# Kernel optimization log

Hardware: AMD Instinct MI355X
Metric: run time of the kernel (lower is better)

## Reference

```python
import jax, jax.numpy as jnp
import numpy as np

M = 8      # number of modalities (len(ModalityType))
D = 256    # embedding_dim
B = 8192   # batch size


def setup_inputs() -> dict:
    key = jax.random.key(0)
    ks = jax.random.split(key, 12)
    s = 1.0 / np.sqrt(D)
    x = jax.random.normal(ks[0], (M, B, D), dtype=jnp.float32)
    reasoning_query = jax.random.normal(ks[1], (B, D), dtype=jnp.float32)
    # Per ordered modality pair (src, tgt): seq_len=1 MHA reduces to out_proj(V_proj(tgt)).
    Wv = jax.random.normal(ks[2], (M, M, D, D), dtype=jnp.float32) * s
    bv = jnp.zeros((M, M, D), dtype=jnp.float32)
    Wo = jax.random.normal(ks[3], (M, M, D, D), dtype=jnp.float32) * s
    bo = jnp.zeros((M, M, D), dtype=jnp.float32)
    # Per-modality fusion MLP: Linear(2D->D), ReLU, Linear(D->D)  (dropout = eval/identity)
    W1 = jax.random.normal(ks[4], (M, D, 2 * D), dtype=jnp.float32) * s
    b1 = jnp.zeros((M, D), dtype=jnp.float32)
    W2 = jax.random.normal(ks[5], (M, D, D), dtype=jnp.float32) * s
    b2 = jnp.zeros((M, D), dtype=jnp.float32)
    # Attention controller: Linear(2D->D), ReLU, Linear(D->1), Sigmoid
    Wc1 = jax.random.normal(ks[6], (D, 2 * D), dtype=jnp.float32) * s
    bc1 = jnp.zeros((D,), dtype=jnp.float32)
    wc2 = jax.random.normal(ks[7], (D,), dtype=jnp.float32) * s
    bc2 = jnp.zeros((1,), dtype=jnp.float32)
    return dict(x=x, reasoning_query=reasoning_query, Wv=Wv, bv=bv, Wo=Wo, bo=bo,
                W1=W1, b1=b1, W2=W2, b2=b2, Wc1=Wc1, bc1=bc1, wc2=wc2, bc2=bc2)


def reference(x, reasoning_query, Wv, bv, Wo, bo, W1, b1, W2, b2, Wc1, bc1, wc2, bc2):
    m = x.shape[0]
    # Cross-modal attention with seq_len=1: softmax over one key == 1, so the
    # attended output is exactly out_proj(V_proj(tgt_embedding)) for every pair.
    h = jnp.einsum('tbd,sted->stbe', x, Wv) + bv[:, :, None, :]          # [M,M,B,D]
    ctx = jnp.einsum('stbe,stoe->stbo', h, Wo) + bo[:, :, None, :]       # [M,M,B,D]
    # Mean over the M-1 target modalities (src != tgt), matching stack(...).mean(-1)
    offdiag = (1.0 - jnp.eye(m, dtype=x.dtype))[:, :, None, None]
    cross = (ctx * offdiag).sum(axis=1) / (m - 1)                         # [M,B,D]
    # Per-modality fusion MLP on cat([original, cross])
    comb = jnp.concatenate([x, cross], axis=-1)                           # [M,B,2D]
    hid = jax.nn.relu(jnp.einsum('mbf,mdf->mbd', comb, W1) + b1[:, None, :])
    fused = jnp.einsum('mbd,mod->mbo', hid, W2) + b2[:, None, :]          # [M,B,D]
    # Reasoning-query gating controller
    q = jnp.broadcast_to(reasoning_query[None], fused.shape)              # [M,B,D]
    qc = jnp.concatenate([q, fused], axis=-1)                             # [M,B,2D]
    ch = jax.nn.relu(jnp.einsum('mbf,df->mbd', qc, Wc1) + bc1)
    score = jax.nn.sigmoid(jnp.einsum('mbd,d->mb', ch, wc2) + bc2)        # [M,B]
    gated = fused * score[..., None]
    unified = gated.mean(axis=0)                                          # [B,D]
    return unified
```

## Files before the change

kernel.cpp:

```cpp
#include <hip/hip_runtime.h>

#define MMOD 8
#define BB 8192
#define DD 256

typedef unsigned short u16;
typedef __attribute__((ext_vector_type(8))) short s16x8;
typedef __attribute__((ext_vector_type(4))) float f32x4;
typedef __attribute__((ext_vector_type(8))) unsigned short u16x8;

typedef __attribute__((address_space(3))) unsigned short lds_u16;
typedef __attribute__((address_space(1))) const unsigned short gl_u16;

__device__ __forceinline__ float b2f(u16 u){ union{unsigned i; float f;} x; x.i=((unsigned)u)<<16; return x.f; }
__device__ __forceinline__ u16 f2b(float f){ union{float f; unsigned i;} x; x.f=f; unsigned r = x.i + 0x7FFF + ((x.i>>16)&1u); return (u16)(r>>16); }

__device__ __forceinline__ void async_cp16(const u16* g, u16* l){
  __builtin_amdgcn_global_load_lds((gl_u16*)g, (lds_u16*)l, 16, 0, 0);
}

struct ConvArgs {
  const float* src[10];
  u16*         dst[10];
  int          n[10];
};
__global__ void convert_kernel(ConvArgs a){
  const long long stride = (long long)gridDim.x * blockDim.x;
  const long long base   = (long long)blockIdx.x * blockDim.x + threadIdx.x;
  for (int s = 0; s < 10; s++){
    const int n  = a.n[s];
    const int n8 = n >> 3;
    const float* sp = a.src[s];
    u16* dst = a.dst[s];
    for (long long i = base; i < n8; i += stride){
      float4 lo = ((const float4*)sp)[i*2];
      float4 hi = ((const float4*)sp)[i*2+1];
      u16x8 p;
      p[0]=f2b(lo.x); p[1]=f2b(lo.y); p[2]=f2b(lo.z); p[3]=f2b(lo.w);
      p[4]=f2b(hi.x); p[5]=f2b(hi.y); p[6]=f2b(hi.z); p[7]=f2b(hi.w);
      *(u16x8*)(dst + (i<<3)) = p;
    }
    for (long long i = ((long long)n8<<3) + base; i < n; i += stride)
      dst[i] = f2b(sp[i]);
  }
}

__device__ __forceinline__ s16x8 load8_f32(const float* p, long long idx){
  float4 lo = *(const float4*)(p + idx);
  float4 hi = *(const float4*)(p + idx + 4);
  s16x8 r;
  r[0]=(short)f2b(lo.x); r[1]=(short)f2b(lo.y); r[2]=(short)f2b(lo.z); r[3]=(short)f2b(lo.w);
  r[4]=(short)f2b(hi.x); r[5]=(short)f2b(hi.y); r[6]=(short)f2b(hi.z); r[7]=(short)f2b(hi.w);
  return r;
}

struct GArgs {
  const u16* A;  long long a_z; long long a_piece; int lda;
  const u16* A2; long long a2_z;
  const u16* B;  long long b_z; int ldb;
  u16*       C;  long long c_z; long long c_npiece; int ldc;
  const u16* bias; long long bias_z;
  const float* cbias;
  const u16* addm;
  const u16* wc2;
  float*     scores;
  float scale;
  int K;
  int relu;
};

__global__ __launch_bounds__(256, 2) void gemm_bt(GArgs g){
  alignas(16) __shared__ u16 lA[128*64];
  alignas(16) __shared__ u16 lB[128*64];
  const int tid  = threadIdx.x;
  const int lane = tid & 63;
  const int w    = tid >> 6;
  const int z    = blockIdx.z;

  const u16* Bbase = g.B + (long long)z * g.b_z + (long long)(blockIdx.y * 128) * g.ldb;

  f32x4 acc[4][4];
  #pragma unroll
  for (int i=0;i<4;i++)
    #pragma unroll
    for (int j=0;j<4;j++)
      #pragma unroll
      for (int r=0;r<4;r++) acc[i][j][r] = 0.0f;

  const int wr = (w >> 1) * 64, wc = (w & 1) * 64;
  const int fm = lane & 15;
  const int fk = (lane >> 4) * 8;
  const long long arow0 = (long long)blockIdx.x * 128;

  const int sr = lane >> 3;
  const int sq = (lane & 7) ^ sr;

  for (int k0 = 0; k0 < g.K; k0 += 64){
    const u16* Abase0 = (g.A2 && k0 >= 256) ? (g.A2 + (long long)z * g.a2_z)
                                            : (g.A  + (long long)z * g.a_z);
    const u16* At = Abase0 + (long long)(k0 >> 8) * g.a_piece + (k0 & 255);
    const u16* Bt = Bbase + k0;
    __syncthreads();
    #pragma unroll
    for (int i=0;i<4;i++){
      int r = i*32 + w*8 + sr;
      async_cp16(At + (arow0 + r) * (long long)g.lda + sq*8, lA + (i*256 + w*64) * 8);
      async_cp16(Bt + (long long)r * g.ldb + sq*8, lB + (i*256 + w*64) * 8);
    }
    __syncthreads();
    #pragma unroll
    for (int kk = 0; kk < 64; kk += 32){
      s16x8 af[4], bfr[4];
      const int qf = (kk + fk) >> 3;
      #pragma unroll
      for (int mi=0; mi<4; mi++){
        int r = wr + mi*16 + fm;
        af[mi] = *(const s16x8*)(lA + (r*8 + (qf ^ (r & 7))) * 8);
      }
      #pragma unroll
      for (int ni=0; ni<4; ni++){
        int r = wc + ni*16 + fm;
        bfr[ni] = *(const s16x8*)(lB + (r*8 + (qf ^ (r & 7))) * 8);
      }
      #pragma unroll
      for (int mi=0; mi<4; mi++)
        #pragma unroll
        for (int ni=0; ni<4; ni++)
          acc[mi][ni] = __builtin_amdgcn_mfma_f32_16x16x32_bf16(af[mi], bfr[ni], acc[mi][ni], 0, 0, 0);
    }
  }

  u16* Cb = g.C + (long long)z * g.c_z;
  const u16* biasp = g.bias ? g.bias + (long long)z * g.bias_z : (const u16*)0;
  #pragma unroll
  for (int mi=0; mi<4; mi++){
    #pragma unroll
    for (int ni=0; ni<4; ni++){
      int n = blockIdx.y*128 + wc + ni*16 + fm;
      float bb = 0.0f;
      if (g.cbias) bb = g.cbias[n];
      else if (biasp) bb = b2f(biasp[n]);
      long long cn = ((long long)(n >> 8)) * g.c_npiece + (n & 255);
      #pragma unroll
      for (int r=0; r<4; r++){
        long long b = arow0 + wr + mi*16 + (lane>>4)*4 + r;
        float v = acc[mi][ni][r] * g.scale + bb;
        if (g.addm) v += b2f(g.addm[b*256 + n]);
        if (g.relu) v = v > 0.0f ? v : 0.0f;
        Cb[cn + b * (long long)g.ldc] = f2b(v);
      }
    }
  }
}

__global__ __launch_bounds__(256, 4) void gemm_thin(GArgs g){
  alignas(16) __shared__ u16 lA[64*64];
  alignas(16) __shared__ u16 lB[256*64];
  const int tid  = threadIdx.x;
  const int lane = tid & 63;
  const int w    = tid >> 6;
  const int z    = blockIdx.z;

  const u16* Bbase = g.B + (long long)z * g.b_z;

  f32x4 acc[16];
  #pragma unroll
  for (int j=0;j<16;j++)
    #pragma unroll
    for (int r=0;r<4;r++) acc[j][r] = 0.0f;

  const int fm = lane & 15;
  const int fk = (lane >> 4) * 8;
  const long long arow0 = (long long)blockIdx.x * 64;

  const int sr = lane >> 3;
  const int sq = (lane & 7) ^ sr;

  for (int k0 = 0; k0 < g.K; k0 += 64){
    const u16* Abase0 = (g.A2 && k0 >= 256) ? (g.A2 + (long long)z * g.a2_z)
                                            : (g.A  + (long long)z * g.a_z);
    const u16* At = Abase0 + (long long)(k0 >> 8) * g.a_piece + (k0 & 255);
    const u16* Bt = Bbase + k0;
    __syncthreads();
    #pragma unroll
    for (int i=0;i<2;i++){
      int r = i*32 + w*8 + sr;
      async_cp16(At + (arow0 + r) * (long long)g.lda + sq*8, lA + (i*256 + w*64) * 8);
    }
    #pragma unroll
    for (int i=0;i<8;i++){
      int r = i*32 + w*8 + sr;
      async_cp16(Bt + (long long)r * g.ldb + sq*8, lB + (i*256 + w*64) * 8);
    }
    __syncthreads();
    #pragma unroll
    for (int kk = 0; kk < 64; kk += 32){
      const int qf = (kk + fk) >> 3;
      int ra = w*16 + fm;
      s16x8 af = *(const s16x8*)(lA + (ra*8 + (qf ^ (ra & 7))) * 8);
      #pragma unroll
      for (int ni=0; ni<16; ni++){
        int r = ni*16 + fm;
        s16x8 bfr = *(const s16x8*)(lB + (r*8 + (qf ^ (r & 7))) * 8);
        acc[ni] = __builtin_amdgcn_mfma_f32_16x16x32_bf16(af, bfr, acc[ni], 0, 0, 0);
      }
    }
  }

  u16* Cb = g.C + (long long)z * g.c_z;
  const u16* biasp = g.bias ? g.bias + (long long)z * g.bias_z : (const u16*)0;
  #pragma unroll
  for (int ni=0; ni<16; ni++){
    int n = ni*16 + fm;
    float bb = 0.0f;
    if (g.cbias) bb = g.cbias[n];
    else if (biasp) bb = b2f(biasp[n]);
    #pragma unroll
    for (int r=0; r<4; r++){
      long long b = arow0 + w*16 + (lane>>4)*4 + r;
      float v = acc[ni][r] * g.scale + bb;
      if (g.addm) v += b2f(g.addm[b*256 + n]);
      if (g.relu) v = v > 0.0f ? v : 0.0f;
      Cb[b * (long long)g.ldc + n] = f2b(v);
    }
  }
}

__global__ __launch_bounds__(256, 4) void gemm_score(GArgs g){
  alignas(16) __shared__ u16 lA[64*64];
  alignas(16) __shared__ u16 lB[256*64];
  const int tid  = threadIdx.x;
  const int lane = tid & 63;
  const int w    = tid >> 6;
  const int z    = blockIdx.z;

  const u16* Bbase = g.B;

  f32x4 acc[16];
  #pragma unroll
  for (int j=0;j<16;j++)
    #pragma unroll
    for (int r=0;r<4;r++) acc[j][r] = 0.0f;

  const int fm = lane & 15;
  const int fk = (lane >> 4) * 8;
  const long long arow0 = (long long)blockIdx.x * 64;

  const int sr = lane >> 3;
  const int sq = (lane & 7) ^ sr;

  for (int k0 = 0; k0 < g.K; k0 += 64){
    const u16* At = g.A + (long long)z * g.a_z + k0;
    const u16* Bt = Bbase + k0;
    __syncthreads();
    #pragma unroll
    for (int i=0;i<2;i++){
      int r = i*32 + w*8 + sr;
      async_cp16(At + (arow0 + r) * (long long)g.lda + sq*8, lA + (i*256 + w*64) * 8);
    }
    #pragma unroll
    for (int i=0;i<8;i++){
      int r = i*32 + w*8 + sr;
      async_cp16(Bt + (long long)r * g.ldb + sq*8, lB + (i*256 + w*64) * 8);
    }
    __syncthreads();
    #pragma unroll
    for (int kk = 0; kk < 64; kk += 32){
      const int qf = (kk + fk) >> 3;
      int ra = w*16 + fm;
      s16x8 af = *(const s16x8*)(lA + (ra*8 + (qf ^ (ra & 7))) * 8);
      #pragma unroll
      for (int ni=0; ni<16; ni++){
        int r = ni*16 + fm;
        s16x8 bfr = *(const s16x8*)(lB + (r*8 + (qf ^ (r & 7))) * 8);
        acc[ni] = __builtin_amdgcn_mfma_f32_16x16x32_bf16(af, bfr, acc[ni], 0, 0, 0);
      }
    }
  }

  float p[4] = {0.f, 0.f, 0.f, 0.f};
  #pragma unroll
  for (int ni=0; ni<16; ni++){
    int n = ni*16 + fm;
    float bb = b2f(g.bias[n]);
    float wcv = b2f(g.wc2[n]);
    #pragma unroll
    for (int r=0; r<4; r++){
      long long b = arow0 + w*16 + (lane>>4)*4 + r;
      float v = acc[ni][r] + bb + b2f(g.addm[b*256 + n]);
      v = v > 0.0f ? v : 0.0f;
      p[r] += v * wcv;
    }
  }
  #pragma unroll
  for (int r=0; r<4; r++){
    #pragma unroll
    for (int off=1; off<16; off<<=1) p[r] += __shfl_xor(p[r], off);
  }
  if (fm == 0){
    float bc2f = g.cbias[0];
    #pragma unroll
    for (int r=0; r<4; r++){
      long long b = arow0 + w*16 + (lane>>4)*4 + r;
      g.scores[(long long)z*BB + b] = 1.0f / (1.0f + __expf(-(p[r] + bc2f)));
    }
  }
}

__global__ __launch_bounds__(256, 2) void build_wb(const float* Wo, const float* Wv, u16* WB){
  alignas(16) __shared__ u16 lA[128*64];
  alignas(16) __shared__ u16 lB[128*64];
  const int tid  = threadIdx.x;
  const int lane = tid & 63;
  const int w    = tid >> 6;
  const int z = blockIdx.z, s = z >> 3, t = z & 7;
  const long long zoff = (long long)z * 65536;

  f32x4 acc[4][4];
  #pragma unroll
  for (int i=0;i<4;i++)
    #pragma unroll
    for (int j=0;j<4;j++)
      #pragma unroll
      for (int r=0;r<4;r++) acc[i][j][r] = 0.0f;

  const int wr = (w >> 1) * 64, wc = (w & 1) * 64;
  const int fm = lane & 15;
  const int fk = (lane >> 4) * 8;

  int srow[4], sq[4];
  #pragma unroll
  for (int i=0;i<4;i++){
    int c = i*256 + tid;
    srow[i] = c >> 3;
    sq[i]   = (c & 7) ^ (srow[i] & 7);
  }

  for (int k0 = 0; k0 < 256; k0 += 64){
    s16x8 va[4], vt[4];
    #pragma unroll
    for (int i=0;i<4;i++){
      long long aidx = zoff + (long long)(blockIdx.x*128 + srow[i]) * 256 + k0 + sq[i]*8;
      va[i] = load8_f32(Wo, aidx);
    }
    #pragma unroll
    for (int j=0;j<4;j++){
      int id = j*256 + tid;
      int e  = id >> 4;
      int dc = (id & 15) * 8;
      long long bidx = zoff + (long long)(k0 + e) * 256 + blockIdx.y*128 + dc;
      vt[j] = load8_f32(Wv, bidx);
    }
    __syncthreads();
    #pragma unroll
    for (int i=0;i<4;i++){
      int c = i*256 + tid;
      *(s16x8*)(lA + c*8) = va[i];
    }
    #pragma unroll
    for (int j=0;j<4;j++){
      int id = j*256 + tid;
      int e  = id >> 4;
      int dc = (id & 15) * 8;
      #pragma unroll
      for (int u=0; u<8; u++){
        int d = dc + u;
        lB[(d*8 + ((e>>3) ^ (d & 7)))*8 + (e & 7)] = (u16)vt[j][u];
      }
    }
    __syncthreads();
    #pragma unroll
    for (int kk = 0; kk < 64; kk += 32){
      s16x8 af[4], bfr[4];
      const int qf = (kk + fk) >> 3;
      #pragma unroll
      for (int mi=0; mi<4; mi++){
        int r = wr + mi*16 + fm;
        af[mi] = *(const s16x8*)(lA + (r*8 + (qf ^ (r & 7))) * 8);
      }
      #pragma unroll
      for (int ni=0; ni<4; ni++){
        int r = wc + ni*16 + fm;
        bfr[ni] = *(const s16x8*)(lB + (r*8 + (qf ^ (r & 7))) * 8);
      }
      #pragma unroll
      for (int mi=0; mi<4; mi++)
        #pragma unroll
        for (int ni=0; ni<4; ni++)
          acc[mi][ni] = __builtin_amdgcn_mfma_f32_16x16x32_bf16(af[mi], bfr[ni], acc[mi][ni], 0, 0, 0);
    }
    __syncthreads();
  }
  const int diag = (s == t);
  #pragma unroll
  for (int mi=0; mi<4; mi++){
    #pragma unroll
    for (int ni=0; ni<4; ni++){
      int d = blockIdx.y*128 + wc + ni*16 + fm;
      #pragma unroll
      for (int r=0; r<4; r++){
        int o = blockIdx.x*128 + wr + mi*16 + (lane>>4)*4 + r;
        float v = diag ? 0.0f : acc[mi][ni][r];
        WB[(long long)(s*256 + o) * 2048 + t*256 + d] = f2b(v);
      }
    }
  }
}

__global__ __launch_bounds__(256) void cb_kernel(const float* bv, const float* Wo, const float* bo, float* cb){
  int z = blockIdx.x, s = z >> 3, t = z & 7;
  if (s == t) return;
  int lane = threadIdx.x & 63, w = threadIdx.x >> 6;
  float4 bvv = *(const float4*)(bv + (long long)z*256 + lane*4);
  #pragma unroll
  for (int i=0; i<16; i++){
    int row = blockIdx.y*64 + w*16 + i;
    float4 wv4 = *(const float4*)(Wo + (long long)z*65536 + (long long)row*256 + lane*4);
    float p = wv4.x*bvv.x + wv4.y*bvv.y + wv4.z*bvv.z + wv4.w*bvv.w;
    #pragma unroll
    for (int off=32; off>0; off>>=1) p += __shfl_xor(p, off);
    if (lane == 0)
      atomicAdd(&cb[s*256 + row], (p + bo[(long long)z*256 + row]) * (1.0f/7.0f));
  }
}

__global__ __launch_bounds__(256) void final_gate(const u16* fused, const float* scores, float* out){
  int b = blockIdx.x;
  int tid = threadIdx.x;
  float sc[8];
  #pragma unroll
  for (int m=0; m<8; m++) sc[m] = scores[(long long)m*BB + b];
  float acc = 0.0f;
  #pragma unroll
  for (int m=0; m<8; m++)
    acc += b2f(fused[((long long)m*BB + b)*256 + tid]) * sc[m];
  out[(long long)b*256 + tid] = acc * 0.125f;
}

extern "C" void kernel_launch(void* const* d_in, const int* in_sizes, int n_in,
                              void* d_out, int out_size, void* d_ws, size_t ws_size,
                              hipStream_t stream){
  const float* x   = (const float*)d_in[0];
  const float* q   = (const float*)d_in[1];
  const float* Wv  = (const float*)d_in[2];
  const float* bv  = (const float*)d_in[3];
  const float* Wo  = (const float*)d_in[4];
  const float* bo  = (const float*)d_in[5];
  const float* W1  = (const float*)d_in[6];
  const float* b1  = (const float*)d_in[7];
  const float* W2  = (const float*)d_in[8];
  const float* b2  = (const float*)d_in[9];
  const float* Wc1 = (const float*)d_in[10];
  const float* bc1 = (const float*)d_in[11];
  const float* wc2 = (const float*)d_in[12];
  const float* bc2 = (const float*)d_in[13];

  char* ws = (char*)d_ws;
  u16*   xb    = (u16*)(ws + 0LL);
  u16*   qb    = (u16*)(ws + 33554432LL);
  u16*   cross = (u16*)(ws + 37748736LL);
  u16*   hid   = (u16*)(ws + 71303168LL);
  u16*   WB    = (u16*)(ws + 104857600LL);
  u16*   W1b   = (u16*)(ws + 113246208LL);
  u16*   W2b   = (u16*)(ws + 115343360LL);
  u16*   Wc1b  = (u16*)(ws + 116391936LL);
  u16*   b1b   = (u16*)(ws + 116654080LL);
  u16*   b2b   = (u16*)(ws + 116658176LL);
  u16*   bc1b  = (u16*)(ws + 116662272LL);
  u16*   wc2b  = (u16*)(ws + 116662784LL);
  float* bc2f  = (float*)(ws + 116663296LL);
  float* cb    = (float*)(ws + 116663424LL);
  u16*   fused = xb;
  u16*   qctx  = WB;
  float* scores = (float*)(ws + 104857600LL + 4194304LL);

  ConvArgs ca{};
  ca.src[0]=x;   ca.dst[0]=xb;   ca.n[0]=MMOD*BB*DD;
  ca.src[1]=q;   ca.dst[1]=qb;   ca.n[1]=BB*DD;
  ca.src[2]=W1;  ca.dst[2]=W1b;  ca.n[2]=MMOD*DD*2*DD;
  ca.src[3]=W2;  ca.dst[3]=W2b;  ca.n[3]=MMOD*DD*DD;
  ca.src[4]=Wc1; ca.dst[4]=Wc1b; ca.n[4]=DD*2*DD;
  ca.src[5]=b1;  ca.dst[5]=b1b;  ca.n[5]=MMOD*DD;
  ca.src[6]=b2;  ca.dst[6]=b2b;  ca.n[6]=MMOD*DD;
  ca.src[7]=bc1; ca.dst[7]=bc1b; ca.n[7]=DD;
  ca.src[8]=wc2; ca.dst[8]=wc2b; ca.n[8]=DD;
  ca.src[9]=bc2; ca.dst[9]=bc1b; ca.n[9]=0;
  convert_kernel<<<1024, 256, 0, stream>>>(ca);
  hipMemcpyAsync(bc2f, bc2, sizeof(float), hipMemcpyDeviceToDevice, stream);

  hipMemsetAsync(cb, 0, 2048*sizeof(float), stream);
  build_wb<<<dim3(2,2,64), 256, 0, stream>>>(Wo, Wv, WB);
  cb_kernel<<<dim3(64,4), 256, 0, stream>>>(bv, Wo, bo, cb);

  const long long BD = (long long)BB * DD;

  GArgs g2{};
  g2.A = xb; g2.a_z = 0; g2.a_piece = BD; g2.lda = 256; g2.A2 = 0; g2.a2_z = 0;
  g2.B = WB; g2.b_z = 0; g2.ldb = 2048;
  g2.C = cross; g2.c_z = 0; g2.c_npiece = BD; g2.ldc = 256;
  g2.bias = 0; g2.bias_z = 0; g2.cbias = cb; g2.addm = 0; g2.wc2 = 0; g2.scores = 0;
  g2.scale = 1.0f/7.0f; g2.K = 2048; g2.relu = 0;
  gemm_bt<<<dim3(64,16,1), 256, 0, stream>>>(g2);

  GArgs g5a{};
  g5a.A = qb; g5a.a_z = 0; g5a.a_piece = 0; g5a.lda = 256; g5a.A2 = 0; g5a.a2_z = 0;
  g5a.B = Wc1b; g5a.b_z = 0; g5a.ldb = 512;
  g5a.C = qctx; g5a.c_z = 0; g5a.c_npiece = 0; g5a.ldc = 256;
  g5a.bias = 0; g5a.bias_z = 0; g5a.cbias = 0; g5a.addm = 0; g5a.wc2 = 0; g5a.scores = 0;
  g5a.scale = 1.0f; g5a.K = 256; g5a.relu = 0;
  gemm_thin<<<dim3(128,1,1), 256, 0, stream>>>(g5a);

  GArgs g3{};
  g3.A = xb; g3.a_z = BD; g3.a_piece = 0; g3.lda = 256; g3.A2 = cross; g3.a2_z = BD;
  g3.B = W1b; g3.b_z = (long long)DD*2*DD; g3.ldb = 512;
  g3.C = hid; g3.c_z = BD; g3.c_npiece = 0; g3.ldc = 256;
  g3.bias = b1b; g3.bias_z = 256; g3.cbias = 0; g3.addm = 0; g3.wc2 = 0; g3.scores = 0;
  g3.scale = 1.0f; g3.K = 512; g3.relu = 1;
  gemm_thin<<<dim3(128,1,8), 256, 0, stream>>>(g3);

  GArgs g4{};
  g4.A = hid; g4.a_z = BD; g4.a_piece = 0; g4.lda = 256; g4.A2 = 0; g4.a2_z = 0;
  g4.B = W2b; g4.b_z = (long long)DD*DD; g4.ldb = 256;
  g4.C = fused; g4.c_z = BD; g4.c_npiece = 0; g4.ldc = 256;
  g4.bias = b2b; g4.bias_z = 256; g4.cbias = 0; g4.addm = 0; g4.wc2 = 0; g4.scores = 0;
  g4.scale = 1.0f; g4.K = 256; g4.relu = 0;
  gemm_thin<<<dim3(128,1,8), 256, 0, stream>>>(g4);

  GArgs g5b{};
  g5b.A = fused; g5b.a_z = BD; g5b.a_piece = 0; g5b.lda = 256; g5b.A2 = 0; g5b.a2_z = 0;
  g5b.B = Wc1b + 256; g5b.b_z = 0; g5b.ldb = 512;
  g5b.C = 0; g5b.c_z = 0; g5b.c_npiece = 0; g5b.ldc = 0;
  g5b.bias = bc1b; g5b.bias_z = 0; g5b.cbias = bc2f; g5b.addm = qctx;
  g5b.wc2 = wc2b; g5b.scores = scores;
  g5b.scale = 1.0f; g5b.K = 256; g5b.relu = 1;
  gemm_score<<<dim3(128,1,8), 256, 0, stream>>>(g5b);

  final_gate<<<dim3(BB), 256, 0, stream>>>(fused, scores, (float*)d_out);

  (void)in_sizes; (void)n_in; (void)out_size; (void)ws_size;
}
```

Measured before the change: 357.2 us.

## Add 256x256-tile 8-wave pipelined GEMM for the cross-modal projection

Adds a new GEMM kernel with 512 threads and 256x256 output tiles. It double-buffers A and B in 128KB of LDS using async global-to-LDS copies, an XOR swizzle, prefetch interleaved across four compute phases, and s_setprio around the MFMA bursts. The kernel replaces gemm_bt for the large K=2048 cross-modal GEMM, aiming for more data reuse per tile and better overlap of loads with MFMA. In exchange it launches only 256 blocks, so wave occupancy is low, and the barrier-heavy schedule may stall.

```diff
diff --git a/kernel.cpp b/kernel.cpp
--- a/kernel.cpp
+++ b/kernel.cpp
@@ -153,6 +153,138 @@
   }
 }
 
+__global__ __launch_bounds__(512, 2) void gemm_8ph(GArgs g){
+  alignas(16) __shared__ u16 L[65536];
+  const int tid  = threadIdx.x;
+  const int lane = tid & 63;
+  const int w    = tid >> 6;
+  const int z    = blockIdx.z;
+
+  const int wr  = w >> 2;
+  const int wcn = w & 3;
+  const int fm  = lane & 15;
+  const int fq  = lane >> 4;
+
+  const long long arow0 = (long long)blockIdx.x * 256;
+  const long long nrow0 = (long long)blockIdx.y * 256;
+
+  const int r0  = tid >> 3;
+  const int r1  = r0 + 64;
+  const int cs  = tid & 7;
+  const int gc0 = cs ^ (r0 & 7);
+  const int gc1 = cs ^ (r1 & 7);
+  const int ldst0 = (w * 64) * 8;
+  const int ldst1 = (512 + w * 64) * 8;
+
+  const u16* Az = g.A + (long long)z * g.a_z;
+  const u16* Bz = g.B + (long long)z * g.b_z;
+
+#define STAGE_A8(c, k0s, h) do{ \
+    const u16* gb_ = Az + (long long)((k0s) >> 8) * g.a_piece + ((k0s) & 255); \
+    const long long gr_ = arow0 + (h) * 128; \
+    u16* lb_ = L + ((c) * 2 + 0) * 16384 + (h) * 8192; \
+    async_cp16(gb_ + (gr_ + r0) * (long long)g.lda + gc0 * 8, lb_ + ldst0); \
+    async_cp16(gb_ + (gr_ + r1) * (long long)g.lda + gc1 * 8, lb_ + ldst1); \
+  }while(0)
+#define STAGE_B8(c, k0s, h) do{ \
+    const u16* gb_ = Bz + (k0s); \
+    const long long gr_ = nrow0 + (h) * 128; \
+    u16* lb_ = L + ((c) * 2 + 1) * 16384 + (h) * 8192; \
+    async_cp16(gb_ + (gr_ + r0) * (long long)g.ldb + gc0 * 8, lb_ + ldst0); \
+    async_cp16(gb_ + (gr_ + r1) * (long long)g.ldb + gc1 * 8, lb_ + ldst1); \
+  }while(0)
+
+  f32x4 acc[8][4];
+  #pragma unroll
+  for (int i=0;i<8;i++)
+    #pragma unroll
+    for (int j=0;j<4;j++)
+      #pragma unroll
+      for (int r=0;r<4;r++) acc[i][j][r] = 0.0f;
+
+  const int T = g.K >> 6;
+
+  STAGE_A8(0, 0, 0);  STAGE_A8(0, 0, 1);
+  STAGE_B8(0, 0, 0);  STAGE_B8(0, 0, 1);
+  STAGE_B8(1, 64, 0); STAGE_B8(1, 64, 1);
+  asm volatile("s_waitcnt vmcnt(4)" ::: "memory");
+  __builtin_amdgcn_s_barrier();
+
+  int c = 0;
+  for (int t = 0; t < T; ++t, c ^= 1){
+    const int k0 = t << 6;
+    const u16* lA = L + (c * 2 + 0) * 16384;
+    const u16* lB = L + (c * 2 + 1) * 16384;
+    s16x8 bf[4][2];
+    #pragma unroll
+    for (int q = 0; q < 4; ++q){
+      if (q == 0 && t + 1 < T) STAGE_A8(c ^ 1, k0 + 64, 0);
+      if (q == 1 && t + 1 < T) STAGE_A8(c ^ 1, k0 + 64, 1);
+      if (q == 2 && t + 2 < T) STAGE_B8(c,     k0 + 128, 0);
+      if (q == 3 && t + 2 < T) STAGE_B8(c,     k0 + 128, 1);
+      if (q == 0){
+        #pragma unroll
+        for (int ni = 0; ni < 4; ni++){
+          const int R = wcn * 64 + ni * 16 + fm;
+          #pragma unroll
+          for (int kk = 0; kk < 2; kk++){
+            const int qf = kk * 4 + fq;
+            bf[ni][kk] = *(const s16x8*)(lB + R * 64 + ((qf ^ (R & 7)) << 3));
+          }
+        }
+      }
+      s16x8 af[2][2];
+      #pragma unroll
+      for (int j = 0; j < 2; j++){
+        const int R = wr * 128 + (q * 2 + j) * 16 + fm;
+        #pragma unroll
+        for (int kk = 0; kk < 2; kk++){
+          const int qf = kk * 4 + fq;
+          af[j][kk] = *(const s16x8*)(lA + R * 64 + ((qf ^ (R & 7)) << 3));
+        }
+      }
+      __builtin_amdgcn_s_barrier();
+      __builtin_amdgcn_s_setprio(1);
+      #pragma unroll
+      for (int kk = 0; kk < 2; kk++)
+        #pragma unroll
+        for (int j = 0; j < 2; j++)
+          #pragma unroll
+          for (int ni = 0; ni < 4; ni++)
+            acc[q*2+j][ni] = __builtin_amdgcn_mfma_f32_16x16x32_bf16(af[j][kk], bf[ni][kk], acc[q*2+j][ni], 0, 0, 0);
+      __builtin_amdgcn_s_setprio(0);
+      if (q == 3){
+        if (t + 2 < T)      asm volatile("s_waitcnt vmcnt(4)" ::: "memory");
+        else if (t + 1 < T) asm volatile("s_waitcnt vmcnt(0)" ::: "memory");
+      }
+      __builtin_amdgcn_s_barrier();
+    }
+  }
+
+  u16* Cb = g.C + (long long)z * g.c_z;
+  const u16* biasp = g.bias ? g.bias + (long long)z * g.bias_z : (const u16*)0;
+  #pragma unroll
+  for (int mi = 0; mi < 8; mi++){
+    #pragma unroll
+    for (int ni = 0; ni < 4; ni++){
+      const int n = (int)nrow0 + wcn * 64 + ni * 16 + fm;
+      float bb = 0.0f;
+      if (g.cbias) bb = g.cbias[n];
+      else if (biasp) bb = b2f(biasp[n]);
+      const long long cn = ((long long)(n >> 8)) * g.c_npiece + (n & 255);
+      #pragma unroll
+      for (int r = 0; r < 4; r++){
+        const long long b = arow0 + wr * 128 + mi * 16 + fq * 4 + r;
+        float v = acc[mi][ni][r] * g.scale + bb;
+        if (g.relu) v = v > 0.0f ? v : 0.0f;
+        Cb[cn + b * (long long)g.ldc] = f2b(v);
+      }
+    }
+  }
+#undef STAGE_A8
+#undef STAGE_B8
+}
+
 __global__ __launch_bounds__(256, 4) void gemm_thin(GArgs g){
   alignas(16) __shared__ u16 lA[64*64];
   alignas(16) __shared__ u16 lB[256*64];
@@ -500,7 +632,7 @@
   g2.C = cross; g2.c_z = 0; g2.c_npiece = BD; g2.ldc = 256;
   g2.bias = 0; g2.bias_z = 0; g2.cbias = cb; g2.addm = 0; g2.wc2 = 0; g2.scores = 0;
   g2.scale = 1.0f/7.0f; g2.K = 2048; g2.relu = 0;
-  gemm_bt<<<dim3(64,16,1), 256, 0, stream>>>(g2);
+  gemm_8ph<<<dim3(32,8,1), 512, 0, stream>>>(g2);
 
   GArgs g5a{};
   g5a.A = qb; g5a.a_z = 0; g5a.a_piece = 0; g5a.lda = 256; g5a.A2 = 0; g5a.a2_z = 0;
```

After: 364.6 us. +2.1%, slower.

## Replace cross-modal GEMM with 256x256-tile, 8-wave, double-buffered pipelined kernel

Applied to the files above, without the earlier changes.

Replaces the 128x128-tile gemm_bt used for the big cross-modal GEMM (K=2048) with a 512-thread kernel that computes 256x256 output tiles per block. The new kernel uses 128KB of LDS, double-buffered across k-tiles. Async global-to-LDS loads for the next tile are interleaved with MFMA phases using explicit vmcnt waits, barriers and s_setprio. The aim is to hide load latency and raise data reuse per block. In exchange the kernel hardcodes lda=256, ldb=2048 and z=0, drops the addm path, and launches only 256 blocks, which may leave some CUs underused.

```diff
diff --git a/kernel.cpp b/kernel.cpp
--- a/kernel.cpp
+++ b/kernel.cpp
@@ -69,88 +69,165 @@
   int relu;
 };
 
-__global__ __launch_bounds__(256, 2) void gemm_bt(GArgs g){
-  alignas(16) __shared__ u16 lA[128*64];
-  alignas(16) __shared__ u16 lB[128*64];
+__global__ __launch_bounds__(512, 2) void gemm_8ph(GArgs g){
+  alignas(16) __shared__ char L[131072];
   const int tid  = threadIdx.x;
   const int lane = tid & 63;
   const int w    = tid >> 6;
-  const int z    = blockIdx.z;
-
-  const u16* Bbase = g.B + (long long)z * g.b_z + (long long)(blockIdx.y * 128) * g.ldb;
-
-  f32x4 acc[4][4];
-  #pragma unroll
-  for (int i=0;i<4;i++)
+
+  const int wr  = w >> 2;
+  const int wcn = w & 3;
+  const int fm  = lane & 15;
+  const int fq  = lane >> 4;
+
+  const long long arow0 = (long long)blockIdx.x * 256;
+  const long long nrow0 = (long long)blockIdx.y * 256;
+
+  const int lp0 = fm*128 + (((0*4+fq) ^ (fm&7))*16);
+  const int lp1 = fm*128 + (((1*4+fq) ^ (fm&7))*16);
+  const int vA00 =          wr*16384 + lp0;
+  const int vA01 =          wr*16384 + lp1;
+  const int vA10 = 65536 +  wr*16384 + lp0;
+  const int vA11 = 65536 +  wr*16384 + lp1;
+  const int vB00 =          32768 + wcn*8192 + lp0;
+  const int vB01 =          32768 + wcn*8192 + lp1;
+  const int vB10 = 65536 +  32768 + wcn*8192 + lp0;
+  const int vB11 = 65536 +  32768 + wcn*8192 + lp1;
+
+  const int r0  = tid >> 3;
+  const int r1  = r0 + 64;
+  const int cs  = tid & 7;
+  const int gc0 = cs ^ (r0 & 7);
+  const int gc1 = cs ^ (r1 & 7);
+  const int laA0 = r0*256  + gc0*8;
+  const int laA1 = r1*256  + gc1*8;
+  const int laB0 = r0*2048 + gc0*8;
+  const int laB1 = r1*2048 + gc1*8;
+
+  const u16* Az = g.A;
+  const u16* Bz = g.B;
+
+#define STAGE_A(c, k0s, h) do{ \
+    const u16* s_ = Az + (long long)((k0s) >> 8) * g.a_piece + ((k0s) & 255) + (arow0 + (h)*128) * 256; \
+    char* d_ = L + (c)*65536 + (h)*16384 + w*1024; \
+    async_cp16(s_ + laA0, (u16*)d_); \
+    async_cp16(s_ + laA1, (u16*)(d_ + 8192)); \
+  }while(0)
+#define STAGE_B(c, k0s, h) do{ \
+    const u16* s_ = Bz + (k0s) + (nrow0 + (h)*128) * 2048; \
+    char* d_ = L + (c)*65536 + 32768 + (h)*16384 + w*1024; \
+    async_cp16(s_ + laB0, (u16*)d_); \
+    async_cp16(s_ + laB1, (u16*)(d_ + 8192)); \
+  }while(0)
+
+  s16x8 af[2][2][2];
+  s16x8 bf[4][2];
+
+#define RD_A(vb0, vb1, slot, qq) do{ \
+    af[slot][0][0] = *(const s16x8*)(L + (vb0) + ((qq)*2+0)*2048); \
+    af[slot][0][1] = *(const s16x8*)(L + (vb1) + ((qq)*2+0)*2048); \
+    af[slot][1][0] = *(const s16x8*)(L + (vb0) + ((qq)*2+1)*2048); \
+    af[slot][1][1] = *(const s16x8*)(L + (vb1) + ((qq)*2+1)*2048); \
+  }while(0)
+#define RD_B(vb0, vb1) do{ \
+    bf[0][0] = *(const s16x8*)(L + (vb0) + 0*2048); \
+    bf[0][1] = *(const s16x8*)(L + (vb1) + 0*2048); \
+    bf[1][0] = *(const s16x8*)(L + (vb0) + 1*2048); \
+    bf[1][1] = *(const s16x8*)(L + (vb1) + 1*2048); \
+    bf[2][0] = *(const s16x8*)(L + (vb0) + 2*2048); \
+    bf[2][1] = *(const s16x8*)(L + (vb1) + 2*2048); \
+    bf[3][0] = *(const s16x8*)(L + (vb0) + 3*2048); \
+    bf[3][1] = *(const s16x8*)(L + (vb1) + 3*2048); \
+  }while(0)
+
+#define MFMA_Q(qq, slot) do{ \
+    __builtin_amdgcn_s_setprio(1); \
+    _Pragma("unroll") \
+    for (int kk = 0; kk < 2; kk++) \
+      _Pragma("unroll") \
+      for (int j = 0; j < 2; j++) \
+        _Pragma("unroll") \
+        for (int ni = 0; ni < 4; ni++) \
+          acc[(qq)*2+j][ni] = __builtin_amdgcn_mfma_f32_16x16x32_bf16(af[slot][j][kk], bf[ni][kk], acc[(qq)*2+j][ni], 0, 0, 0); \
+    __builtin_amdgcn_s_setprio(0); \
+  }while(0)
+
+  f32x4 acc[8][4];
+  #pragma unroll
+  for (int i=0;i<8;i++)
     #pragma unroll
     for (int j=0;j<4;j++)
       #pragma unroll
       for (int r=0;r<4;r++) acc[i][j][r] = 0.0f;
 
-  const int wr = (w >> 1) * 64, wc = (w & 1) * 64;
-  const int fm = lane & 15;
-  const int fk = (lane >> 4) * 8;
-  const long long arow0 = (long long)blockIdx.x * 128;
-
-  const int sr = lane >> 3;
-  const int sq = (lane & 7) ^ sr;
-
-  for (int k0 = 0; k0 < g.K; k0 += 64){
-    const u16* Abase0 = (g.A2 && k0 >= 256) ? (g.A2 + (long long)z * g.a2_z)
-                                            : (g.A  + (long long)z * g.a_z);
-    const u16* At = Abase0 + (long long)(k0 >> 8) * g.a_piece + (k0 & 255);
-    const u16* Bt = Bbase + k0;
-    __syncthreads();
-    #pragma unroll
-    for (int i=0;i<4;i++){
-      int r = i*32 + w*8 + sr;
-      async_cp16(At + (arow0 + r) * (long long)g.lda + sq*8, lA + (i*256 + w*64) * 8);
-      async_cp16(Bt + (long long)r * g.ldb + sq*8, lB + (i*256 + w*64) * 8);
-    }
-    __syncthreads();
-    #pragma unroll
-    for (int kk = 0; kk < 64; kk += 32){
-      s16x8 af[4], bfr[4];
-      const int qf = (kk + fk) >> 3;
-      #pragma unroll
-      for (int mi=0; mi<4; mi++){
-        int r = wr + mi*16 + fm;
-        af[mi] = *(const s16x8*)(lA + (r*8 + (qf ^ (r & 7))) * 8);
-      }
-      #pragma unroll
-      for (int ni=0; ni<4; ni++){
-        int r = wc + ni*16 + fm;
-        bfr[ni] = *(const s16x8*)(lB + (r*8 + (qf ^ (r & 7))) * 8);
-      }
-      #pragma unroll
-      for (int mi=0; mi<4; mi++)
-        #pragma unroll
-        for (int ni=0; ni<4; ni++)
-          acc[mi][ni] = __builtin_amdgcn_mfma_f32_16x16x32_bf16(af[mi], bfr[ni], acc[mi][ni], 0, 0, 0);
-    }
-  }
-
-  u16* Cb = g.C + (long long)z * g.c_z;
-  const u16* biasp = g.bias ? g.bias + (long long)z * g.bias_z : (const u16*)0;
-  #pragma unroll
-  for (int mi=0; mi<4; mi++){
-    #pragma unroll
-    for (int ni=0; ni<4; ni++){
-      int n = blockIdx.y*128 + wc + ni*16 + fm;
+  const int T = g.K >> 6;
+
+  STAGE_A(0, 0, 0);  STAGE_A(0, 0, 1);
+  STAGE_B(0, 0, 0);  STAGE_B(0, 0, 1);
+  STAGE_B(1, 64, 0); STAGE_B(1, 64, 1);
+  asm volatile("s_waitcnt vmcnt(4)" ::: "memory");
+  __builtin_amdgcn_s_barrier();
+
+#define TILE(c, vAk0, vAk1, vBk0, vBk1, t) do{ \
+    const int kt = (t) << 6; \
+    const int more1 = (t) + 1 < T; \
+    const int more2 = (t) + 2 < T; \
+     \
+    if (more1) STAGE_A((c)^1, kt+64, 0); \
+    RD_B(vBk0, vBk1); \
+    RD_A(vAk0, vAk1, 0, 0); \
+    RD_A(vAk0, vAk1, 1, 1); \
+    MFMA_Q(0, 0); \
+    __builtin_amdgcn_s_barrier(); \
+     \
+    if (more1) STAGE_A((c)^1, kt+64, 1); \
+    RD_A(vAk0, vAk1, 0, 2); \
+    MFMA_Q(1, 1); \
+    __builtin_amdgcn_s_barrier(); \
+     \
+    if (more2) STAGE_B((c), kt+128, 0); \
+    RD_A(vAk0, vAk1, 1, 3); \
+    MFMA_Q(2, 0); \
+    __builtin_amdgcn_s_barrier(); \
+     \
+    if (more2) STAGE_B((c), kt+128, 1); \
+    MFMA_Q(3, 1); \
+    if (more2)      asm volatile("s_waitcnt vmcnt(4)" ::: "memory"); \
+    else if (more1) asm volatile("s_waitcnt vmcnt(0)" ::: "memory"); \
+    __builtin_amdgcn_s_barrier(); \
+  }while(0)
+
+  for (int t = 0; t < T; t += 2){
+    TILE(0, vA00, vA01, vB00, vB01, t);
+    TILE(1, vA10, vA11, vB10, vB11, t+1);
+  }
+
+  u16* Cb = g.C + 0;
+  const u16* biasp = g.bias;
+  #pragma unroll
+  for (int mi = 0; mi < 8; mi++){
+    #pragma unroll
+    for (int ni = 0; ni < 4; ni++){
+      const int n = (int)nrow0 + wcn * 64 + ni * 16 + fm;
       float bb = 0.0f;
       if (g.cbias) bb = g.cbias[n];
       else if (biasp) bb = b2f(biasp[n]);
-      long long cn = ((long long)(n >> 8)) * g.c_npiece + (n & 255);
-      #pragma unroll
-      for (int r=0; r<4; r++){
-        long long b = arow0 + wr + mi*16 + (lane>>4)*4 + r;
+      const long long cn = ((long long)(n >> 8)) * g.c_npiece + (n & 255);
+      #pragma unroll
+      for (int r = 0; r < 4; r++){
+        const long long b = arow0 + wr * 128 + mi * 16 + fq * 4 + r;
         float v = acc[mi][ni][r] * g.scale + bb;
-        if (g.addm) v += b2f(g.addm[b*256 + n]);
         if (g.relu) v = v > 0.0f ? v : 0.0f;
         Cb[cn + b * (long long)g.ldc] = f2b(v);
       }
     }
   }
+#undef STAGE_A
+#undef STAGE_B
+#undef RD_A
+#undef RD_B
+#undef MFMA_Q
+#undef TILE
 }
 
 __global__ __launch_bounds__(256, 4) void gemm_thin(GArgs g){
@@ -500,7 +577,7 @@
   g2.C = cross; g2.c_z = 0; g2.c_npiece = BD; g2.ldc = 256;
   g2.bias = 0; g2.bias_z = 0; g2.cbias = cb; g2.addm = 0; g2.wc2 = 0; g2.scores = 0;
   g2.scale = 1.0f/7.0f; g2.K = 2048; g2.relu = 0;
-  gemm_bt<<<dim3(64,16,1), 256, 0, stream>>>(g2);
+  gemm_8ph<<<dim3(32,8,1), 512, 0, stream>>>(g2);
 
   GArgs g5a{};
   g5a.A = qb; g5a.a_z = 0; g5a.a_piece = 0; g5a.lda = 256; g5a.A2 = 0; g5a.a2_z = 0;
```

Result: no change. 354.3 us (-0.8%).
